# Kernel tuning notes

Measured on AMD Instinct MI355X. Metric: run time of the kernel, lower is better.

The kernel has to match this reference:

```python
import jax, jax.numpy as jnp
import numpy as np

PI = float(np.pi)
C = jnp.complex64
N = 10  # qubits

def m2(a, b, c, d):
    a, b, c, d = jnp.broadcast_arrays(*(jnp.asarray(v, C) for v in (a, b, c, d)))
    return jnp.stack([jnp.stack([a, b], -1), jnp.stack([c, d], -1)], -2)

def rx_mat(t):
    c = jnp.cos(t / 2); s = jnp.sin(t / 2)
    return m2(c, -1j * s, -1j * s, c)

def ry_mat(t):
    c = jnp.cos(t / 2); s = jnp.sin(t / 2)
    return m2(c, -s, s, c)

def rz_mat(t):
    return m2(jnp.exp(-0.5j * t), 0.0, 0.0, jnp.exp(0.5j * t))

def ps_mat(t):
    return m2(1.0, 0.0, 0.0, jnp.exp(1j * t))

def rot_mat(phi, theta, omega):
    c = jnp.cos(theta / 2); s = jnp.sin(theta / 2)
    return m2(jnp.exp(-0.5j * (phi + omega)) * c,
              -jnp.exp(0.5j * (phi - omega)) * s,
              jnp.exp(-0.5j * (phi - omega)) * s,
              jnp.exp(0.5j * (phi + omega)) * c)

def u2_mat(phi, lam):
    r = 1.0 / np.sqrt(2.0)
    return m2(r, -r * jnp.exp(1j * lam), r * jnp.exp(1j * phi), r * jnp.exp(1j * (phi + lam)))

def u3_mat(theta, phi, lam):
    c = jnp.cos(theta / 2); s = jnp.sin(theta / 2)
    return m2(c, -jnp.exp(1j * lam) * s, jnp.exp(1j * phi) * s, jnp.exp(1j * (phi + lam)) * c)

def controlled(U):
    sh = U.shape[:-2]
    I2 = jnp.broadcast_to(jnp.eye(2, dtype=C), sh + (2, 2))
    Z2 = jnp.zeros(sh + (2, 2), C)
    return jnp.concatenate([jnp.concatenate([I2, Z2], -1), jnp.concatenate([Z2, U], -1)], -2)

Y_M = jnp.array([[0, -1j], [1j, 0]], C)
S_M = jnp.array([[1, 0], [0, 1j]], C)
T_M = jnp.array([[1, 0], [0, np.exp(1j * np.pi / 4)]], C)
SX_M = 0.5 * jnp.array([[1 + 1j, 1 - 1j], [1 - 1j, 1 + 1j]], C)
CNOT_M = jnp.array(np.eye(4)[[0, 1, 3, 2]], C)
CZ_M = jnp.array(np.diag([1.0, 1.0, 1.0, -1.0]), C)
CY_M = jnp.array([[1, 0, 0, 0], [0, 1, 0, 0], [0, 0, 0, -1j], [0, 0, 1j, 0]], C)
SWAP_M = jnp.array(np.eye(4)[[0, 2, 1, 3]], C)
CSWAP_M = jnp.array(np.eye(8)[[0, 1, 2, 3, 4, 6, 5, 7]], C)
TOFF_M = jnp.array(np.eye(8)[[0, 1, 2, 3, 4, 5, 7, 6]], C)
CX12_M = jnp.array(np.eye(4)[[0, 1, 3, 2]], C)  # qubitunitary [[1,0,0,0],[0,1,0,0],[0,0,0,1],[0,0,1,0]]

def apply_gate(state, U, wires):
    # state: [B] + [2]*N ; U: [2^k,2^k] or [B,2^k,2^k]
    B = state.shape[0]
    k = len(wires)
    axes = tuple(w + 1 for w in wires)
    s = jnp.moveaxis(state, axes, tuple(range(1, 1 + k)))
    sh = s.shape
    s = s.reshape(B, 2 ** k, -1)
    U = jnp.asarray(U, s.dtype)
    if U.ndim == 2:
        s = jnp.einsum('ij,bjr->bir', U, s)
    else:
        s = jnp.einsum('bij,bjr->bir', U, s)
    return jnp.moveaxis(s.reshape(sh), tuple(range(1, 1 + k)), axes)

def multirz(state, theta, wires):
    # diagonal exp(-i theta/2 * Z...Z) phase
    z = jnp.array([1.0, -1.0], jnp.float32)
    sign = jnp.ones((1,) * (N + 1), jnp.float32)
    for w in wires:
        shp = [1] * (N + 1); shp[w + 1] = 2
        sign = sign * z.reshape(shp)
    theta = jnp.reshape(jnp.asarray(theta), (-1,) + (1,) * N)
    return state * jnp.exp(-0.5j * theta * sign)

def net(x, w1, b1, w2, b2, fw1, fb1, fw2, fb2):
    dn = ('NCHW', 'OIHW', 'NCHW')
    h = jax.lax.conv_general_dilated(x, w1, (1, 1), 'VALID', dimension_numbers=dn)
    h = jax.nn.relu(h + b1[None, :, None, None])
    h = jax.lax.conv_general_dilated(h, w2, (1, 1), 'VALID', dimension_numbers=dn)
    h = jax.nn.relu(h + b2[None, :, None, None])
    h = jax.lax.reduce_window(h, -jnp.inf, jax.lax.max, (1, 1, 2, 2), (1, 1, 2, 2), 'VALID')
    h = h.reshape(h.shape[0], -1)  # [B, 9216]
    h = jax.nn.relu(h @ fw1.T + fb1)
    h = h @ fw2.T + fb2
    return jax.nn.sigmoid(h) * (2.0 * PI)  # angles in [0, 2pi], dropout in eval mode

def run_circuit(ang, q_rx, q_rz3, q_ps6, q_rot7, q_mrz8, q_crx9, q_cry10, q_crz11, q_u2, q_u3):
    B = ang.shape[0]
    state = jnp.zeros((B, 2 ** N), C).at[:, 0].set(1.0).reshape((B,) + (2,) * N)
    for k in range(N):  # TrainableOpAll(RX)
        state = apply_gate(state, rx_mat(q_rx[k]), (k,))
    for k in range(N):  # OpAll(RY) + repeated rx(wire0, x[:,0])
        state = apply_gate(state, ry_mat(ang[:, k]), (k,))
        state = apply_gate(state, rx_mat(ang[:, 0]), (0,))
    for k in range(N - 1):  # TQAll CNOT ring
        state = apply_gate(state, CNOT_M, (k, k + 1))
    state = apply_gate(state, CNOT_M, (N - 1, 0))
    state = apply_gate(state, rx_mat(ang[:, 1]), (1,))
    state = apply_gate(state, rx_mat(jnp.float32(-PI / 4)), (5,))  # q_layer2 fixed
    state = apply_gate(state, ry_mat(ang[:, 2]), (2,))
    state = apply_gate(state, rz_mat(ang[:, 3]), (3,))
    state = apply_gate(state, S_M, (4,))
    state = apply_gate(state, T_M, (5,))
    state = apply_gate(state, rz_mat(q_rz3[0]), (6,))
    state = apply_gate(state, SX_M, (7,))
    # q_device1 (3-wire) ops do not affect the output -> omitted
    state = apply_gate(state, CZ_M, (0, 5))
    state = apply_gate(state, CNOT_M, (0, 5))
    state = apply_gate(state, CY_M, (0, 5))
    state = apply_gate(state, CY_M, (3, 8))
    state = apply_gate(state, SWAP_M, (2, 3))
    state = apply_gate(state, CSWAP_M, (4, 5, 6))
    state = apply_gate(state, TOFF_M, (8, 5, 0))
    state = apply_gate(state, ps_mat(q_ps6[0]), (8,))
    state = apply_gate(state, ps_mat(ang[:, 7]), (7,))
    state = apply_gate(state, rot_mat(q_rot7[0], q_rot7[1], q_rot7[2]), (4,))
    state = apply_gate(state, rot_mat(ang[:, 6], ang[:, 7], ang[:, 8]), (5,))
    state = multirz(state, q_mrz8[0], (2, 3, 4, 5, 6))
    state = multirz(state, ang[:, 5], (3, 4, 6, 7, 8))
    state = apply_gate(state, controlled(rx_mat(ang[:, 6])), (0, 1))
    state = apply_gate(state, controlled(rx_mat(q_crx9[0])), (4, 5))
    state = apply_gate(state, controlled(ry_mat(ang[:, 6])), (0, 1))
    state = apply_gate(state, controlled(ry_mat(q_cry10[0])), (4, 5))
    state = apply_gate(state, controlled(rz_mat(ang[:, 6])), (0, 1))
    state = apply_gate(state, controlled(rz_mat(q_crz11[0])), (4, 5))
    state = apply_gate(state, controlled(rot_mat(jnp.float32(-PI / 4), jnp.float32(PI / 4), jnp.float32(PI / 2))), (5, 6))
    state = apply_gate(state, controlled(rot_mat(ang[:, 5], ang[:, 6], ang[:, 7])), (7, 8))
    state = apply_gate(state, ps_mat(jnp.float32(PI / 7)), (1,))  # U1 == PhaseShift
    state = apply_gate(state, ps_mat(ang[:, 9]), (2,))
    state = apply_gate(state, u2_mat(q_u2[0], q_u2[1]), (8,))
    state = apply_gate(state, u2_mat(ang[:, 0], ang[:, 1]), (4,))
    state = apply_gate(state, u3_mat(q_u3[0], q_u3[1], q_u3[2]), (5,))
    state = apply_gate(state, u3_mat(ang[:, 4], ang[:, 5], ang[:, 6]), (5,))
    # q_layer16 QubitUnitary is identity -> no-op
    state = apply_gate(state, CX12_M, (1, 2))
    red = tuple(range(1, N + 1))
    evs = [jnp.real(jnp.sum(jnp.conj(state) * apply_gate(state, Y_M, (w,)), axis=red)) for w in range(N)]
    return jnp.stack(evs, 1)  # [B, 10]

def setup_inputs():
    key = jax.random.key(0)
    ks = jax.random.split(key, 16)
    B = 1024
    return {
        'x': jax.random.uniform(ks[0], (B, 1, 28, 28), jnp.float32),
        'conv1_w': jax.random.normal(ks[1], (32, 1, 3, 3), jnp.float32) * 0.2,
        'conv1_b': jnp.zeros((32,), jnp.float32),
        'conv2_w': jax.random.normal(ks[2], (64, 32, 3, 3), jnp.float32) * 0.05,
        'conv2_b': jnp.zeros((64,), jnp.float32),
        'fc1_w': jax.random.normal(ks[3], (128, 9216), jnp.float32) * 0.01,
        'fc1_b': jnp.zeros((128,), jnp.float32),
        'fc2_w': jax.random.normal(ks[4], (10, 128), jnp.float32) * 0.08,
        'fc2_b': jnp.zeros((10,), jnp.float32),
        'q_rx': jax.random.uniform(ks[5], (10,), jnp.float32, 0.0, 2 * PI),
        'q_rz3': jax.random.uniform(ks[6], (1,), jnp.float32, 0.0, 2 * PI),
        'q_ps6': jax.random.uniform(ks[7], (1,), jnp.float32, 0.0, 2 * PI),
        'q_rot7': jax.random.uniform(ks[8], (3,), jnp.float32, 0.0, 2 * PI),
        'q_mrz8': jax.random.uniform(ks[9], (1,), jnp.float32, 0.0, 2 * PI),
        'q_crx9': jax.random.uniform(ks[10], (1,), jnp.float32, 0.0, 2 * PI),
        'q_cry10': jax.random.uniform(ks[11], (1,), jnp.float32, 0.0, 2 * PI),
        'q_crz11': jax.random.uniform(ks[12], (1,), jnp.float32, 0.0, 2 * PI),
        'q_u2_14': jnp.array([PI / 7, PI / 8.8], jnp.float32),
        'q_u3_15': jax.random.uniform(ks[13], (3,), jnp.float32, 0.0, 2 * PI),
    }

def reference(x, conv1_w, conv1_b, conv2_w, conv2_b, fc1_w, fc1_b, fc2_w, fc2_b,
              q_rx, q_rz3, q_ps6, q_rot7, q_mrz8, q_crx9, q_cry10, q_crz11, q_u2_14, q_u3_15):
    ang = net(x, conv1_w, conv1_b, conv2_w, conv2_b, fc1_w, fc1_b, fc2_w, fc2_b)
    ev = run_circuit(ang, q_rx, q_rz3, q_ps6, q_rot7, q_mrz8, q_crx9, q_cry10, q_crz11, q_u2_14, q_u3_15)
    return jax.nn.log_softmax(ev, axis=1)
```

## Files before the change

kernel.cpp:

```cpp
#include <hip/hip_runtime.h>
#include <hip/hip_bf16.h>

#define PI_F 3.14159265358979323846f

__global__ void Static_82300163326800_kernel() {}

typedef _Float16 f16x8 __attribute__((ext_vector_type(8)));
typedef _Float16 f16x4 __attribute__((ext_vector_type(4)));
typedef float f32x4 __attribute__((ext_vector_type(4)));

struct M2 { float2 m00, m01, m10, m11; };

__device__ __forceinline__ float2 cmul2(float2 a, float2 b) {
    return make_float2(a.x*b.x - a.y*b.y, a.x*b.y + a.y*b.x);
}
__device__ __forceinline__ float2 cadd2(float2 a, float2 b) {
    return make_float2(a.x+b.x, a.y+b.y);
}
__device__ __forceinline__ float2 shx(float2 v, int m) {
    return make_float2(__shfl_xor(v.x, m), __shfl_xor(v.y, m));
}
__device__ __forceinline__ M2 m2mul(M2 b, M2 a) {
    return { cadd2(cmul2(b.m00,a.m00), cmul2(b.m01,a.m10)),
             cadd2(cmul2(b.m00,a.m01), cmul2(b.m01,a.m11)),
             cadd2(cmul2(b.m10,a.m00), cmul2(b.m11,a.m10)),
             cadd2(cmul2(b.m10,a.m01), cmul2(b.m11,a.m11)) };
}
__device__ __forceinline__ M2 mrx(float th) {
    float s, c; __sincosf(0.5f * th, &s, &c);
    return { make_float2(c,0.f), make_float2(0.f,-s), make_float2(0.f,-s), make_float2(c,0.f) };
}
__device__ __forceinline__ M2 mry(float th) {
    float s, c; __sincosf(0.5f * th, &s, &c);
    return { make_float2(c,0.f), make_float2(-s,0.f), make_float2(s,0.f), make_float2(c,0.f) };
}
__device__ __forceinline__ M2 mrot(float phi, float th, float om) {
    float s, c;  __sincosf(0.5f * th, &s, &c);
    float sa, ca; __sincosf(0.5f * (phi + om), &sa, &ca);
    float sd, cd; __sincosf(0.5f * (phi - om), &sd, &cd);
    return { make_float2(ca*c, -sa*c), make_float2(-cd*s, -sd*s),
             make_float2(cd*s, -sd*s), make_float2(ca*c,  sa*c) };
}
__device__ __forceinline__ M2 mu2(float phi, float lam) {
    const float r = 0.7071067811865476f;
    float sl, cl;   __sincosf(lam, &sl, &cl);
    float sp, cp;   __sincosf(phi, &sp, &cp);
    float spl, cpl; __sincosf(phi + lam, &spl, &cpl);
    return { make_float2(r,0.f), make_float2(-r*cl,-r*sl),
             make_float2(r*cp, r*sp), make_float2(r*cpl, r*spl) };
}
__device__ __forceinline__ M2 mu3(float th, float phi, float lam) {
    float s, c;     __sincosf(0.5f * th, &s, &c);
    float sl, cl;   __sincosf(lam, &sl, &cl);
    float sp, cp;   __sincosf(phi, &sp, &cp);
    float spl, cpl; __sincosf(phi + lam, &spl, &cpl);
    return { make_float2(c,0.f), make_float2(-cl*s,-sl*s),
             make_float2(cp*s, sp*s), make_float2(cpl*c, spl*c) };
}


__device__ __forceinline__ void applyL(float2* s, M2 m, int lane, int q) {
    const int bitv = (lane >> q) & 1;
    const float2 cA = bitv ? m.m11 : m.m00;
    const float2 cB = bitv ? m.m10 : m.m01;
    float ox[16], oy[16];
#pragma unroll
    for (int r = 0; r < 16; ++r) {
        ox[r] = __shfl_xor(s[r].x, 1 << q);
        oy[r] = __shfl_xor(s[r].y, 1 << q);
    }
#pragma unroll
    for (int r = 0; r < 16; ++r)
        s[r] = make_float2(cA.x*s[r].x - cA.y*s[r].y + cB.x*ox[r] - cB.y*oy[r],
                           cA.x*s[r].y + cA.y*s[r].x + cB.x*oy[r] + cB.y*ox[r]);
}
template<int P>
__device__ __forceinline__ void applyR(float2* s, M2 m) {
#pragma unroll
    for (int r0 = 0; r0 < 16; ++r0) {
        if (r0 & (1 << P)) continue;
        const int r1 = r0 | (1 << P);
        float2 a = s[r0], d = s[r1];
        s[r0] = cadd2(cmul2(m.m00, a), cmul2(m.m01, d));
        s[r1] = cadd2(cmul2(m.m10, a), cmul2(m.m11, d));
    }
}
__device__ __forceinline__ void diagL(float2* s, float2 d0, float2 d1, int lane, int q) {
    const int bitv = (lane >> q) & 1;
    const float2 f = bitv ? d1 : d0;
#pragma unroll
    for (int r = 0; r < 16; ++r) s[r] = cmul2(f, s[r]);
}
template<int P>
__device__ __forceinline__ void diagR(float2* s, float2 d0, float2 d1) {
#pragma unroll
    for (int r = 0; r < 16; ++r) {
        const float2 f = (r & (1 << P)) ? d1 : d0;
        s[r] = cmul2(f, s[r]);
    }
}
__device__ __forceinline__ void cnotLL(float2* s, int lane, int qc, int qw) {
    const int cb = (lane >> qc) & 1;
    float ox[16], oy[16];
#pragma unroll
    for (int r = 0; r < 16; ++r) {
        ox[r] = __shfl_xor(s[r].x, 1 << qw);
        oy[r] = __shfl_xor(s[r].y, 1 << qw);
    }
#pragma unroll
    for (int r = 0; r < 16; ++r)
        s[r] = cb ? make_float2(ox[r], oy[r]) : s[r];
}
__device__ __forceinline__ void capplyLL(float2* s, M2 m, int lane, int qc, int qw) {
    const int cb = (lane >> qc) & 1, tb = (lane >> qw) & 1;
    float2 cA = tb ? m.m11 : m.m00;
    float2 cB = tb ? m.m10 : m.m01;
    cA = cb ? cA : make_float2(1.f, 0.f);
    cB = cb ? cB : make_float2(0.f, 0.f);
    float ox[16], oy[16];
#pragma unroll
    for (int r = 0; r < 16; ++r) {
        ox[r] = __shfl_xor(s[r].x, 1 << qw);
        oy[r] = __shfl_xor(s[r].y, 1 << qw);
    }
#pragma unroll
    for (int r = 0; r < 16; ++r)
        s[r] = make_float2(cA.x*s[r].x - cA.y*s[r].y + cB.x*ox[r] - cB.y*oy[r],
                           cA.x*s[r].y + cA.y*s[r].x + cB.x*oy[r] + cB.y*ox[r]);
}
__device__ __forceinline__ void cdiagLL(float2* s, float2 d0, float2 d1, int lane, int qc, int qw) {
    const int cb = (lane >> qc) & 1, tb = (lane >> qw) & 1;
    float2 f = tb ? d1 : d0;
    f = cb ? f : make_float2(1.f, 0.f);
#pragma unroll
    for (int r = 0; r < 16; ++r) s[r] = cmul2(f, s[r]);
}
template<int P>
__device__ __forceinline__ void capplyRL(float2* s, M2 m, int lane, int qc) {
    const int cb = (lane >> qc) & 1;
#pragma unroll
    for (int r0 = 0; r0 < 16; ++r0) {
        if (r0 & (1 << P)) continue;
        const int r1 = r0 | (1 << P);
        float2 a = s[r0], d = s[r1];
        float2 na = cadd2(cmul2(m.m00, a), cmul2(m.m01, d));
        float2 nd = cadd2(cmul2(m.m10, a), cmul2(m.m11, d));
        s[r0] = cb ? na : a;
        s[r1] = cb ? nd : d;
    }
}

__global__ __launch_bounds__(256, 1) void circuit_wave(
    const float* __restrict__ ang_g,
    const float* __restrict__ q_rx, const float* __restrict__ q_rz3,
    const float* __restrict__ q_ps6, const float* __restrict__ q_rot7,
    const float* __restrict__ q_mrz8, const float* __restrict__ q_crx9,
    const float* __restrict__ q_cry10, const float* __restrict__ q_crz11,
    const float* __restrict__ q_u2, const float* __restrict__ q_u3,
    float* __restrict__ out)
{
    const int t = threadIdx.x, lane = t & 63, wv = t >> 6;
    const int b = blockIdx.x * 4 + wv;
    float ang[10];
#pragma unroll
    for (int j = 0; j < 10; ++j) ang[j] = ang_g[b * 10 + j];

    float2 s[16];
#pragma unroll
    for (int r = 0; r < 16; ++r) s[r] = make_float2(0.f, 0.f);
    if (lane == 0) s[0].x = 1.f;

    applyL(s, mrx(q_rx[0]), lane, 5);
    applyL(s, mrx(q_rx[1]), lane, 4);
    applyL(s, mrx(q_rx[2]), lane, 3);
    applyL(s, mrx(q_rx[3]), lane, 2);
    applyL(s, mrx(q_rx[4]), lane, 1);
    applyL(s, mrx(q_rx[5]), lane, 0);
    applyR<3>(s, mrx(q_rx[6]));
    applyR<2>(s, mrx(q_rx[7]));
    applyR<1>(s, mrx(q_rx[8]));
    applyR<0>(s, mrx(q_rx[9]));
    applyL(s, mry(ang[0]), lane, 5);
    applyL(s, mry(ang[1]), lane, 4);
    applyL(s, mry(ang[2]), lane, 3);
    applyL(s, mry(ang[3]), lane, 2);
    applyL(s, mry(ang[4]), lane, 1);
    applyL(s, mry(ang[5]), lane, 0);
    applyR<3>(s, mry(ang[6]));
    applyR<2>(s, mry(ang[7]));
    applyR<1>(s, mry(ang[8]));
    applyR<0>(s, mry(ang[9]));
    applyL(s, mrx(10.f * ang[0]), lane, 5);
    cnotLL(s, lane, 5, 4);
    cnotLL(s, lane, 4, 3);
    cnotLL(s, lane, 3, 2);
    cnotLL(s, lane, 2, 1);
    cnotLL(s, lane, 1, 0);
    {
        const int cb = lane & 1;
#pragma unroll
        for (int r0 = 0; r0 < 8; ++r0) {
            float2 a = s[r0], d = s[r0 + 8];
            s[r0] = cb ? d : a; s[r0 + 8] = cb ? a : d;
        }
    }
    {
        float2 u;
        u = s[8];  s[8]  = s[12]; s[12] = u;
        u = s[9];  s[9]  = s[13]; s[13] = u;
        u = s[10]; s[10] = s[14]; s[14] = u;
        u = s[11]; s[11] = s[15]; s[15] = u;
    }
    {
        float2 u;
        u = s[4];  s[4]  = s[6];  s[6]  = u;
        u = s[5];  s[5]  = s[7];  s[7]  = u;
        u = s[12]; s[12] = s[14]; s[14] = u;
        u = s[13]; s[13] = s[15]; s[15] = u;
    }
    {
        float2 u;
        u = s[2];  s[2]  = s[3];  s[3]  = u;
        u = s[6];  s[6]  = s[7];  s[7]  = u;
        u = s[10]; s[10] = s[11]; s[11] = u;
        u = s[14]; s[14] = s[15]; s[15] = u;
    }
    {
        float ox[8], oy[8];
#pragma unroll
        for (int k = 0; k < 8; ++k) {
            ox[k] = __shfl_xor(s[2*k+1].x, 32);
            oy[k] = __shfl_xor(s[2*k+1].y, 32);
        }
#pragma unroll
        for (int k = 0; k < 8; ++k) s[2*k+1] = make_float2(ox[k], oy[k]);
    }

    applyL(s, mrx(ang[1]), lane, 4);
    applyL(s, mrx(-PI_F / 4.f), lane, 0);
    applyL(s, mry(ang[2]), lane, 3);
    { float sn, cs; __sincosf(0.5f * ang[3], &sn, &cs);
      diagL(s, make_float2(cs,-sn), make_float2(cs,sn), lane, 2); }
    diagL(s, make_float2(1.f,0.f), make_float2(0.f,1.f), lane, 1);
    diagL(s, make_float2(1.f,0.f),
          make_float2(0.7071067811865476f, 0.7071067811865476f), lane, 0);
    { float sn, cs; __sincosf(0.5f * q_rz3[0], &sn, &cs);
      diagR<3>(s, make_float2(cs,-sn), make_float2(cs,sn)); }
    { M2 m = { make_float2(0.5f,0.5f), make_float2(0.5f,-0.5f),
               make_float2(0.5f,-0.5f), make_float2(0.5f,0.5f) };
      applyR<2>(s, m); }
    {
        const int cb = (lane >> 5) & 1;
#pragma unroll
        for (int r = 0; r < 16; ++r)
            s[r] = cb ? make_float2(s[r].y, -s[r].x) : s[r];
    }
    {
        const int cb = (lane >> 2) & 1;
#pragma unroll
        for (int r0 = 0; r0 < 16; ++r0) {
            if (r0 & 2) continue;
            const int r1 = r0 | 2;
            float2 a = s[r0], d = s[r1];
            float2 na = make_float2(d.y, -d.x);
            float2 nd = make_float2(-a.y, a.x);
            s[r0] = cb ? na : a; s[r1] = cb ? nd : d;
        }
    }
    {
        const int pr = ((lane >> 3) & 1) ^ ((lane >> 2) & 1);
        float ox[16], oy[16];
#pragma unroll
        for (int r = 0; r < 16; ++r) {
            ox[r] = __shfl_xor(s[r].x, 12);
            oy[r] = __shfl_xor(s[r].y, 12);
        }
#pragma unroll
        for (int r = 0; r < 16; ++r)
            s[r] = pr ? make_float2(ox[r], oy[r]) : s[r];
    }
    {
        float ox[16], oy[16];
#pragma unroll
        for (int r = 0; r < 16; ++r) {
            ox[r] = __shfl_xor(s[r ^ 8].x, 1);
            oy[r] = __shfl_xor(s[r ^ 8].y, 1);
        }
        const int cb = (lane >> 1) & 1, lb = lane & 1;
#pragma unroll
        for (int r = 0; r < 16; ++r) {
            const int pr = cb & ((r & 8) ? (1 - lb) : lb);
            s[r] = pr ? make_float2(ox[r], oy[r]) : s[r];
        }
    }
    {
        const int lb = lane & 1;
        float ox[8], oy[8];
        const int idx8[8] = {2,3,6,7,10,11,14,15};
#pragma unroll
        for (int k = 0; k < 8; ++k) {
            ox[k] = __shfl_xor(s[idx8[k]].x, 32);
            oy[k] = __shfl_xor(s[idx8[k]].y, 32);
        }
#pragma unroll
        for (int k = 0; k < 8; ++k)
            s[idx8[k]] = lb ? make_float2(ox[k], oy[k]) : s[idx8[k]];
    }
    { float sn, cs; __sincosf(q_ps6[0], &sn, &cs);
      diagR<1>(s, make_float2(1.f,0.f), make_float2(cs,sn)); }
    { float sn, cs; __sincosf(ang[7], &sn, &cs);
      diagR<2>(s, make_float2(1.f,0.f), make_float2(cs,sn)); }
    applyL(s, mrot(q_rot7[0], q_rot7[1], q_rot7[2]), lane, 1);
    applyL(s, mrot(ang[6], ang[7], ang[8]), lane, 0);
    {
        float sh, ch; __sincosf(0.5f * q_mrz8[0], &sh, &ch);
        const int lp = __popc(lane & 0xF) & 1;
        const float sg0 = lp ? sh : -sh;
#pragma unroll
        for (int r = 0; r < 16; ++r) {
            const float sg = (r & 8) ? -sg0 : sg0;
            float2 a = s[r];
            s[r] = make_float2(ch*a.x - sg*a.y, ch*a.y + sg*a.x);
        }
    }
    {
        float sh, ch; __sincosf(0.5f * ang[5], &sh, &ch);
        const int lp = __popc(lane & 6) & 1;
        const float sg0 = lp ? sh : -sh;
#pragma unroll
        for (int r = 0; r < 16; ++r) {
            const int rp = __popc(r & 14) & 1;
            const float sg = rp ? -sg0 : sg0;
            float2 a = s[r];
            s[r] = make_float2(ch*a.x - sg*a.y, ch*a.y + sg*a.x);
        }
    }
    capplyLL(s, mrx(ang[6]), lane, 5, 4);
    capplyLL(s, mrx(q_crx9[0]), lane, 1, 0);
    capplyLL(s, mry(ang[6]), lane, 5, 4);
    capplyLL(s, mry(q_cry10[0]), lane, 1, 0);
    { float sn, cs; __sincosf(0.5f * ang[6], &sn, &cs);
      cdiagLL(s, make_float2(cs,-sn), make_float2(cs,sn), lane, 5, 4); }
    { float sn, cs; __sincosf(0.5f * q_crz11[0], &sn, &cs);
      cdiagLL(s, make_float2(cs,-sn), make_float2(cs,sn), lane, 1, 0); }
    capplyRL<3>(s, mrot(-PI_F/4.f, PI_F/4.f, PI_F/2.f), lane, 0);
    {
        M2 m = mrot(ang[5], ang[6], ang[7]);
        const int idx4[4] = {4, 5, 12, 13};
#pragma unroll
        for (int k = 0; k < 4; ++k) {
            const int r0 = idx4[k], r1 = r0 | 2;
            float2 a = s[r0], d = s[r1];
            s[r0] = cadd2(cmul2(m.m00, a), cmul2(m.m01, d));
            s[r1] = cadd2(cmul2(m.m10, a), cmul2(m.m11, d));
        }
    }
    { float sn, cs; __sincosf(PI_F / 7.f, &sn, &cs);
      diagL(s, make_float2(1.f,0.f), make_float2(cs,sn), lane, 4); }
    { float sn, cs; __sincosf(ang[9], &sn, &cs);
      diagL(s, make_float2(1.f,0.f), make_float2(cs,sn), lane, 3); }
    applyR<1>(s, mu2(q_u2[0], q_u2[1]));
    applyL(s, mu2(ang[0], ang[1]), lane, 1);
    applyL(s, m2mul(mu3(ang[4], ang[5], ang[6]),
                    mu3(q_u3[0], q_u3[1], q_u3[2])), lane, 0);
    cnotLL(s, lane, 4, 3);

    float ev[10];
#pragma unroll
    for (int w = 0; w < 6; ++w) {
        const int q = 5 - w;
        const int bitv = (lane >> q) & 1;
        float ox[16], oy[16];
#pragma unroll
        for (int r = 0; r < 16; ++r) {
            ox[r] = __shfl_xor(s[r].x, 1 << q);
            oy[r] = __shfl_xor(s[r].y, 1 << q);
        }
        float acc = 0.f;
#pragma unroll
        for (int r = 0; r < 16; ++r)
            acc += s[r].x * oy[r] - s[r].y * ox[r];
        ev[w] = bitv ? 0.f : 2.f * acc;
    }
#pragma unroll
    for (int w = 6; w < 10; ++w) {
        const int P = 9 - w;
        float acc = 0.f;
#pragma unroll
        for (int r0 = 0; r0 < 16; ++r0) {
            if (r0 & (1 << P)) continue;
            const int r1 = r0 | (1 << P);
            acc += s[r0].x * s[r1].y - s[r0].y * s[r1].x;
        }
        ev[w] = 2.f * acc;
    }
#pragma unroll
    for (int w = 0; w < 10; ++w) {
        float v = ev[w];
        v += __shfl_down(v, 32); v += __shfl_down(v, 16); v += __shfl_down(v, 8);
        v += __shfl_down(v, 4);  v += __shfl_down(v, 2);  v += __shfl_down(v, 1);
        ev[w] = v;
    }
    if (lane == 0) {
        float mx = ev[0];
#pragma unroll
        for (int i = 1; i < 10; ++i) mx = fmaxf(mx, ev[i]);
        float ss = 0.f;
#pragma unroll
        for (int i = 0; i < 10; ++i) ss += expf(ev[i] - mx);
        const float ls = logf(ss);
#pragma unroll
        for (int i = 0; i < 10; ++i) out[b * 10 + i] = ev[i] - mx - ls;
    }
}

__global__ __launch_bounds__(256) void prep_w2(
    const float* __restrict__ w2, _Float16* __restrict__ w2t)
{
    int idx = blockIdx.x * 256 + threadIdx.x;
    if (idx < 18432) {
        int oc = idx / 288, r = idx - oc * 288;
        int s = r >> 5, ic = r & 31;
        w2t[idx] = (_Float16)w2[oc * 288 + ic * 9 + s];
    }
}

__global__ __launch_bounds__(256) void prep_fw1(
    const float* __restrict__ fw1, _Float16* __restrict__ out)
{
    int i = blockIdx.x * 256 + threadIdx.x;
    if (i < 294912) {
        float4 v = ((const float4*)fw1)[i];
        f16x4 o = { (_Float16)v.x, (_Float16)v.y, (_Float16)v.z, (_Float16)v.w };
        *(f16x4*)(out + i * 4) = o;
    }
}

__global__ __launch_bounds__(256, 2) void convnet_mfma(
    const float* __restrict__ x, const float* __restrict__ w1, const float* __restrict__ b1,
    const _Float16* __restrict__ w2t, const float* __restrict__ b2,
    _Float16* __restrict__ flat)
{
    __shared__ float xs[784];
    __shared__ float w1s[288];
    __shared__ __align__(16) _Float16 h1t[676 * 40];
    const int n = blockIdx.x, t = threadIdx.x;
    const int lane = t & 63, wv = t >> 6;
    const int m = lane & 15, quad = lane >> 4;

    for (int i = t; i < 784; i += 256) xs[i] = x[n * 784 + i];
    for (int i = t; i < 288; i += 256) w1s[i] = w1[i];

    f16x8 bq[9][4];
#pragma unroll
    for (int s = 0; s < 9; ++s)
#pragma unroll
        for (int nt = 0; nt < 4; ++nt)
            bq[s][nt] = *(const f16x8*)(w2t + (nt * 16 + m) * 288 + s * 32 + quad * 8);

    __syncthreads();

    {
        const int ic = t & 31, j = t >> 5;
        float wr[9];
#pragma unroll
        for (int k = 0; k < 9; ++k) wr[k] = w1s[ic * 9 + k];
        const float bb = b1[ic];
        for (int pg = j; pg < 13; pg += 8) {
            const int y0 = 2 * pg;
            float p0[4], p1[4];
#pragma unroll
            for (int k = 0; k < 4; ++k) {
                p0[k] = xs[(y0 + k) * 28];
                p1[k] = xs[(y0 + k) * 28 + 1];
            }
            for (int xx = 0; xx < 26; ++xx) {
                float n2[4];
#pragma unroll
                for (int k = 0; k < 4; ++k) n2[k] = xs[(y0 + k) * 28 + xx + 2];
                float s0 = bb, s1 = bb;
#pragma unroll
                for (int ky = 0; ky < 3; ++ky) {
                    s0 += p0[ky] * wr[3*ky] + p1[ky] * wr[3*ky+1] + n2[ky] * wr[3*ky+2];
                    s1 += p0[ky+1] * wr[3*ky] + p1[ky+1] * wr[3*ky+1] + n2[ky+1] * wr[3*ky+2];
                }
                h1t[(y0 * 26 + xx) * 40 + ic]       = (_Float16)fmaxf(s0, 0.f);
                h1t[((y0 + 1) * 26 + xx) * 40 + ic] = (_Float16)fmaxf(s1, 0.f);
#pragma unroll
                for (int k = 0; k < 4; ++k) { p0[k] = p1[k]; p1[k] = n2[k]; }
            }
        }
    }
    __syncthreads();

    float bb2[4];
#pragma unroll
    for (int nt = 0; nt < 4; ++nt) bb2[nt] = b2[nt * 16 + m];

    _Float16* outp = flat + (size_t)n * 9216;

    for (int q = 0; q < 9; ++q) {
        const int mt = wv + q * 4;
        const int a = mt / 3, b3 = mt - a * 3;
        const int y0 = 2 * a + (m & 1), x0 = 8 * b3 + (m >> 1);
        f32x4 acc[4] = {};
#pragma unroll
        for (int s = 0; s < 9; ++s) {
            const int ky = s / 3, kx = s - ky * 3;
            f16x8 af = *(const f16x8*)&h1t[((y0 + ky) * 26 + x0 + kx) * 40 + quad * 8];
#pragma unroll
            for (int nt = 0; nt < 4; ++nt)
                acc[nt] = __builtin_amdgcn_mfma_f32_16x16x32_f16(af, bq[s][nt], acc[nt], 0, 0, 0);
        }
        const int pooled_idx = a * 12 + 4 * b3 + quad;
#pragma unroll
        for (int nt = 0; nt < 4; ++nt) {
            float v = fmaxf(fmaxf(acc[nt][0], acc[nt][1]), fmaxf(acc[nt][2], acc[nt][3]));
            outp[(nt * 16 + m) * 144 + pooled_idx] = (_Float16)fmaxf(v + bb2[nt], 0.f);
        }
    }
}

__global__ __launch_bounds__(256) void fc1_mfma(
    const _Float16* __restrict__ A, const _Float16* __restrict__ B, float* __restrict__ part)
{
    const int m0 = blockIdx.x * 64, n0 = blockIdx.y * 64, kb = blockIdx.z;
    const int t = threadIdx.x, lane = t & 63, wv = t >> 6;
    const int r = lane & 15, quad = lane >> 4;
    const _Float16* ap = A + (size_t)(m0 + wv * 16 + r) * 9216 + kb * 576 + quad * 8;
    const _Float16* bp = B + (size_t)(n0 + r) * 9216 + kb * 576 + quad * 8;
    f32x4 acc[4] = {};
    for (int ks = 0; ks < 576; ks += 32) {
        f16x8 af = *(const f16x8*)(ap + ks);
#pragma unroll
        for (int nt = 0; nt < 4; ++nt) {
            f16x8 bfr = *(const f16x8*)(bp + (size_t)nt * 16 * 9216 + ks);
            acc[nt] = __builtin_amdgcn_mfma_f32_16x16x32_f16(af, bfr, acc[nt], 0, 0, 0);
        }
    }
    float* pp = part + (size_t)kb * 131072 + (size_t)(m0 + wv * 16 + quad * 4) * 128 + n0 + r;
#pragma unroll
    for (int nt = 0; nt < 4; ++nt)
#pragma unroll
        for (int reg = 0; reg < 4; ++reg)
            pp[reg * 128 + nt * 16] = acc[nt][reg];
}

__global__ __launch_bounds__(128) void fc2_kernel(
    const float* __restrict__ part, const float* __restrict__ fb1,
    const float* __restrict__ fw2, const float* __restrict__ fb2, float* __restrict__ angO)
{
    __shared__ float h[128];
    const int b = blockIdx.x, t = threadIdx.x;
    float s = fb1[t];
#pragma unroll
    for (int kb = 0; kb < 16; ++kb) s += part[(size_t)kb * 131072 + b * 128 + t];
    h[t] = fmaxf(s, 0.f);
    __syncthreads();
    if (t < 10) {
        float d = fb2[t];
#pragma unroll 16
        for (int k = 0; k < 128; ++k) d += h[k] * fw2[t * 128 + k];
        angO[b * 10 + t] = 6.283185307179586f / (1.f + expf(-d));
    }
}

__device__ __forceinline__ int ins1(int x, int p) {
    return ((x >> p) << (p + 1)) | (x & ((1 << p) - 1));
}
__device__ __forceinline__ void apply1(float2* st, int t, int w, M2 m) {
    int p = 9 - w;
    int i0 = ins1(t, p), i1 = i0 | (1 << p);
    float2 a = st[i0], d = st[i1];
    st[i0] = cadd2(cmul2(m.m00, a), cmul2(m.m01, d));
    st[i1] = cadd2(cmul2(m.m10, a), cmul2(m.m11, d));
}
__device__ __forceinline__ void diag1(float2* st, int t, int w, float2 d0, float2 d1) {
    int p = 9 - w;
    int i0 = ins1(t, p), i1 = i0 | (1 << p);
    st[i0] = cmul2(d0, st[i0]);
    st[i1] = cmul2(d1, st[i1]);
}
__device__ __forceinline__ void capply1(float2* st, int t, int c, int w, M2 m) {
    if (t < 256) {
        int pc = 9 - c, pw = 9 - w;
        int pl = pc < pw ? pc : pw, ph = pc + pw - pl;
        int base = ins1(ins1(t, pl), ph) | (1 << pc);
        int i0 = base, i1 = base | (1 << pw);
        float2 a = st[i0], d = st[i1];
        st[i0] = cadd2(cmul2(m.m00, a), cmul2(m.m01, d));
        st[i1] = cadd2(cmul2(m.m10, a), cmul2(m.m11, d));
    }
}
__device__ __forceinline__ void cdiag1(float2* st, int t, int c, int w, float2 d0, float2 d1) {
    if (t < 256) {
        int pc = 9 - c, pw = 9 - w;
        int pl = pc < pw ? pc : pw, ph = pc + pw - pl;
        int base = ins1(ins1(t, pl), ph) | (1 << pc);
        st[base] = cmul2(d0, st[base]);
        st[base | (1 << pw)] = cmul2(d1, st[base | (1 << pw)]);
    }
}
__device__ __forceinline__ void cnotg(float2* st, int t, int c, int w) {
    if (t < 256) {
        int pc = 9 - c, pw = 9 - w;
        int pl = pc < pw ? pc : pw, ph = pc + pw - pl;
        int base = ins1(ins1(t, pl), ph) | (1 << pc);
        int i1 = base | (1 << pw);
        float2 a = st[base]; st[base] = st[i1]; st[i1] = a;
    }
}
__device__ __forceinline__ void czg(float2* st, int t, int c, int w) {
    if (t < 256) {
        int pc = 9 - c, pw = 9 - w;
        int pl = pc < pw ? pc : pw, ph = pc + pw - pl;
        int i = ins1(ins1(t, pl), ph) | (1 << pc) | (1 << pw);
        st[i] = make_float2(-st[i].x, -st[i].y);
    }
}
__device__ __forceinline__ void swapg(float2* st, int t, int a, int b_) {
    if (t < 256) {
        int pa = 9 - a, pb = 9 - b_;
        int pl = pa < pb ? pa : pb, ph = pa + pb - pl;
        int base = ins1(ins1(t, pl), ph);
        int iA = base | (1 << pa), iB = base | (1 << pb);
        float2 u = st[iA]; st[iA] = st[iB]; st[iB] = u;
    }
}
__device__ __forceinline__ void cswap456f(float2* st, int t) {
    if (t < 128) {
        int base = ins1(ins1(ins1(t, 3), 4), 5) | (1 << 5);
        int iA = base | (1 << 4), iB = base | (1 << 3);
        float2 u = st[iA]; st[iA] = st[iB]; st[iB] = u;
    }
}
__device__ __forceinline__ void toff850f(float2* st, int t) {
    if (t < 128) {
        int base = ins1(ins1(ins1(t, 1), 4), 9) | (1 << 1) | (1 << 4);
        int i1 = base | (1 << 9);
        float2 u = st[base]; st[base] = st[i1]; st[i1] = u;
    }
}
__device__ __forceinline__ void mrzg(float2* st, int t, int mask, float th) {
    float sh, ch; __sincosf(0.5f * th, &sh, &ch);
#pragma unroll
    for (int q = 0; q < 2; ++q) {
        int i = t + q * 512;
        float sg = (__popc(i & mask) & 1) ? sh : -sh;
        float2 a = st[i];
        st[i] = make_float2(ch*a.x - sg*a.y, ch*a.y + sg*a.x);
    }
}
__device__ __forceinline__ void run_circ(
    float2* st, float (*red)[10], float* evs, int t, const float* ang,
    const float* q_rx, const float* q_rz3, const float* q_ps6, const float* q_rot7,
    const float* q_mrz8, const float* q_crx9, const float* q_cry10, const float* q_crz11,
    const float* q_u2, const float* q_u3, float* outf)
{
    st[t] = make_float2(t == 0 ? 1.f : 0.f, 0.f);
    st[t + 512] = make_float2(0.f, 0.f);
#pragma unroll
    for (int k = 0; k < 10; ++k) { M2 m = mrx(q_rx[k]); __syncthreads(); apply1(st, t, k, m); }
    {
        M2 mx0 = mrx(ang[0]);
#pragma unroll
        for (int k = 0; k < 10; ++k) {
            M2 m = mry(ang[k]); __syncthreads(); apply1(st, t, k, m);
            __syncthreads(); apply1(st, t, 0, mx0);
        }
    }
#pragma unroll
    for (int k = 0; k < 9; ++k) { __syncthreads(); cnotg(st, t, k, k + 1); }
    __syncthreads(); cnotg(st, t, 9, 0);
    { M2 m = mrx(ang[1]);      __syncthreads(); apply1(st, t, 1, m); }
    { M2 m = mrx(-PI_F / 4.f); __syncthreads(); apply1(st, t, 5, m); }
    { M2 m = mry(ang[2]);      __syncthreads(); apply1(st, t, 2, m); }
    { float s, c; __sincosf(0.5f * ang[3], &s, &c);
      __syncthreads(); diag1(st, t, 3, make_float2(c,-s), make_float2(c,s)); }
    __syncthreads(); diag1(st, t, 4, make_float2(1.f,0.f), make_float2(0.f,1.f));
    __syncthreads(); diag1(st, t, 5, make_float2(1.f,0.f),
                           make_float2(0.7071067811865476f, 0.7071067811865476f));
    { float s, c; __sincosf(0.5f * q_rz3[0], &s, &c);
      __syncthreads(); diag1(st, t, 6, make_float2(c,-s), make_float2(c,s)); }
    { M2 m = { make_float2(0.5f,0.5f), make_float2(0.5f,-0.5f),
               make_float2(0.5f,-0.5f), make_float2(0.5f,0.5f) };
      __syncthreads(); apply1(st, t, 7, m); }
    __syncthreads(); czg(st, t, 0, 5);
    __syncthreads(); cnotg(st, t, 0, 5);
    { M2 y = { make_float2(0.f,0.f), make_float2(0.f,-1.f),
               make_float2(0.f,1.f), make_float2(0.f,0.f) };
      __syncthreads(); capply1(st, t, 0, 5, y);
      __syncthreads(); capply1(st, t, 3, 8, y); }
    __syncthreads(); swapg(st, t, 2, 3);
    __syncthreads(); cswap456f(st, t);
    __syncthreads(); toff850f(st, t);
    { float s, c; __sincosf(q_ps6[0], &s, &c);
      __syncthreads(); diag1(st, t, 8, make_float2(1.f,0.f), make_float2(c,s)); }
    { float s, c; __sincosf(ang[7], &s, &c);
      __syncthreads(); diag1(st, t, 7, make_float2(1.f,0.f), make_float2(c,s)); }
    { M2 m = mrot(q_rot7[0], q_rot7[1], q_rot7[2]); __syncthreads(); apply1(st, t, 4, m); }
    { M2 m = mrot(ang[6], ang[7], ang[8]);          __syncthreads(); apply1(st, t, 5, m); }
    __syncthreads(); mrzg(st, t, 0xF8, q_mrz8[0]);
    __syncthreads(); mrzg(st, t, 0x6E, ang[5]);
    { M2 m = mrx(ang[6]);      __syncthreads(); capply1(st, t, 0, 1, m); }
    { M2 m = mrx(q_crx9[0]);   __syncthreads(); capply1(st, t, 4, 5, m); }
    { M2 m = mry(ang[6]);      __syncthreads(); capply1(st, t, 0, 1, m); }
    { M2 m = mry(q_cry10[0]);  __syncthreads(); capply1(st, t, 4, 5, m); }
    { float s, c; __sincosf(0.5f * ang[6], &s, &c);
      __syncthreads(); cdiag1(st, t, 0, 1, make_float2(c,-s), make_float2(c,s)); }
    { float s, c; __sincosf(0.5f * q_crz11[0], &s, &c);
      __syncthreads(); cdiag1(st, t, 4, 5, make_float2(c,-s), make_float2(c,s)); }
    { M2 m = mrot(-PI_F/4.f, PI_F/4.f, PI_F/2.f); __syncthreads(); capply1(st, t, 5, 6, m); }
    { M2 m = mrot(ang[5], ang[6], ang[7]);        __syncthreads(); capply1(st, t, 7, 8, m); }
    { float s, c; __sincosf(PI_F/7.f, &s, &c);
      __syncthreads(); diag1(st, t, 1, make_float2(1.f,0.f), make_float2(c,s)); }
    { float s, c; __sincosf(ang[9], &s, &c);
      __syncthreads(); diag1(st, t, 2, make_float2(1.f,0.f), make_float2(c,s)); }
    { M2 m = mu2(q_u2[0], q_u2[1]); __syncthreads(); apply1(st, t, 8, m); }
    { M2 m = mu2(ang[0], ang[1]);   __syncthreads(); apply1(st, t, 4, m); }
    { M2 m = mu3(q_u3[0], q_u3[1], q_u3[2]); __syncthreads(); apply1(st, t, 5, m); }
    { M2 m = mu3(ang[4], ang[5], ang[6]);    __syncthreads(); apply1(st, t, 5, m); }
    __syncthreads(); cnotg(st, t, 1, 2);
    __syncthreads();
    float loc[10];
#pragma unroll
    for (int w = 0; w < 10; ++w) {
        int p = 9 - w;
        int i0 = ins1(t, p), i1 = i0 | (1 << p);
        float2 a = st[i0], c = st[i1];
        loc[w] = 2.f * (a.x * c.y - a.y * c.x);
    }
    int lane = t & 63, wvv = t >> 6;
#pragma unroll
    for (int w = 0; w < 10; ++w) {
        float v = loc[w];
        v += __shfl_down(v, 32); v += __shfl_down(v, 16); v += __shfl_down(v, 8);
        v += __shfl_down(v, 4);  v += __shfl_down(v, 2);  v += __shfl_down(v, 1);
        if (lane == 0) red[wvv][w] = v;
    }
    __syncthreads();
    if (t < 10) {
        float e = 0.f;
#pragma unroll
        for (int i = 0; i < 8; ++i) e += red[i][t];
        evs[t] = e;
    }
    __syncthreads();
    if (t < 10) {
        float mx = evs[0];
#pragma unroll
        for (int i = 1; i < 10; ++i) mx = fmaxf(mx, evs[i]);
        float ss = 0.f;
#pragma unroll
        for (int i = 0; i < 10; ++i) ss += expf(evs[i] - mx);
        outf[t] = evs[t] - mx - logf(ss);
    }
}
template <int NT>
__device__ __forceinline__ void conv_stage(
    float* buf, int n, int t,
    const float* __restrict__ x, const float* __restrict__ w1, const float* __restrict__ b1,
    const float* __restrict__ w2, const float* __restrict__ b2)
{
    float* xs  = buf;
    float* w1s = buf + 784;
    float* h1s = buf + 1072;
    float* w2s = buf + 1748;
    const int ocq = t / 24, r = t - ocq * 24;
    const bool active = (t < 384);
    for (int i = t; i < 784; i += NT) xs[i] = x[n * 784 + i];
    for (int i = t; i < 288; i += NT) w1s[i] = w1[i];
    float acc[4][24];
#pragma unroll
    for (int j = 0; j < 4; ++j)
#pragma unroll
        for (int xo = 0; xo < 24; ++xo) acc[j][xo] = 0.f;
    for (int ic = 0; ic < 32; ++ic) {
        __syncthreads();
        float bb1 = b1[ic];
        for (int i = t; i < 676; i += NT) {
            int yy = i / 26, xx = i - yy * 26;
            const float* xp = xs + yy * 28 + xx;
            const float* wp = w1s + ic * 9;
            float s = bb1;
#pragma unroll
            for (int ky = 0; ky < 3; ++ky)
#pragma unroll
                for (int kx = 0; kx < 3; ++kx)
                    s += xp[ky * 28 + kx] * wp[ky * 3 + kx];
            h1s[i] = fmaxf(s, 0.f);
        }
        for (int i = t; i < 576; i += NT) {
            int oc = i / 9, k = i - oc * 9;
            w2s[i] = w2[oc * 288 + ic * 9 + k];
        }
        __syncthreads();
        if (active) {
            float wr[4][9];
#pragma unroll
            for (int j = 0; j < 4; ++j)
#pragma unroll
                for (int k = 0; k < 9; ++k)
                    wr[j][k] = w2s[(ocq * 4 + j) * 9 + k];
            float c0[3], c1[3];
#pragma unroll
            for (int q = 0; q < 3; ++q) { c0[q] = h1s[(r + q) * 26]; c1[q] = h1s[(r + q) * 26 + 1]; }
#pragma unroll
            for (int xo = 0; xo < 24; ++xo) {
                float c2[3];
#pragma unroll
                for (int q = 0; q < 3; ++q) c2[q] = h1s[(r + q) * 26 + xo + 2];
#pragma unroll
                for (int j = 0; j < 4; ++j) {
                    acc[j][xo] += wr[j][0]*c0[0] + wr[j][1]*c1[0] + wr[j][2]*c2[0]
                                + wr[j][3]*c0[1] + wr[j][4]*c1[1] + wr[j][5]*c2[1]
                                + wr[j][6]*c0[2] + wr[j][7]*c1[2] + wr[j][8]*c2[2];
                }
#pragma unroll
                for (int q = 0; q < 3; ++q) { c0[q] = c1[q]; c1[q] = c2[q]; }
            }
        }
    }
    __syncthreads();
    if (active && (r & 1)) {
#pragma unroll
        for (int j = 0; j < 4; ++j) {
            int oc = ocq * 4 + j;
            float bb = b2[oc];
#pragma unroll
            for (int px = 0; px < 12; ++px) {
                float v0 = fmaxf(acc[j][2*px]   + bb, 0.f);
                float v1 = fmaxf(acc[j][2*px+1] + bb, 0.f);
                buf[oc * 144 + (r >> 1) * 12 + px] = fmaxf(v0, v1);
            }
        }
    }
    __syncthreads();
    if (active && !(r & 1)) {
#pragma unroll
        for (int j = 0; j < 4; ++j) {
            int oc = ocq * 4 + j;
            float bb = b2[oc];
#pragma unroll
            for (int px = 0; px < 12; ++px) {
                float v0 = fmaxf(acc[j][2*px]   + bb, 0.f);
                float v1 = fmaxf(acc[j][2*px+1] + bb, 0.f);
                int idx = oc * 144 + (r >> 1) * 12 + px;
                buf[idx] = fmaxf(fmaxf(v0, v1), buf[idx]);
            }
        }
    }
    __syncthreads();
}
__global__ __launch_bounds__(512) void fused_kernel(
    const float* __restrict__ x, const float* __restrict__ w1, const float* __restrict__ b1,
    const float* __restrict__ w2, const float* __restrict__ b2,
    const float* __restrict__ fw1, const float* __restrict__ fb1,
    const float* __restrict__ fw2, const float* __restrict__ fb2,
    const float* __restrict__ q_rx, const float* __restrict__ q_rz3,
    const float* __restrict__ q_ps6, const float* __restrict__ q_rot7,
    const float* __restrict__ q_mrz8, const float* __restrict__ q_crx9,
    const float* __restrict__ q_cry10, const float* __restrict__ q_crz11,
    const float* __restrict__ q_u2, const float* __restrict__ q_u3,
    float* __restrict__ out)
{
    __shared__ float buf[9216];
    __shared__ float2 st[1024];
    __shared__ float hred[512];
    __shared__ float hvec[128];
    __shared__ float angs[10];
    __shared__ float red[8][10];
    __shared__ float evs[10];
    const int n = blockIdx.x, t = threadIdx.x;
    conv_stage<512>(buf, n, t, x, w1, b1, w2, b2);
    {
        const int j = t >> 2, q = t & 3;
        const float* wrow = fw1 + (size_t)j * 9216 + q * 2304;
        const float* arow = buf + q * 2304;
        float s = 0.f;
        for (int k = 0; k < 2304; k += 4) {
            float4 w = *(const float4*)(wrow + k);
            s += w.x * arow[k] + w.y * arow[k+1] + w.z * arow[k+2] + w.w * arow[k+3];
        }
        hred[t] = s;
    }
    __syncthreads();
    if (t < 128)
        hvec[t] = fmaxf(fb1[t] + hred[t*4] + hred[t*4+1] + hred[t*4+2] + hred[t*4+3], 0.f);
    __syncthreads();
    if (t < 10) {
        float d = fb2[t];
#pragma unroll 16
        for (int k = 0; k < 128; ++k) d += hvec[k] * fw2[t * 128 + k];
        angs[t] = 6.283185307179586f / (1.f + expf(-d));
    }
    __syncthreads();
    run_circ(st, red, evs, t, angs, q_rx, q_rz3, q_ps6, q_rot7, q_mrz8,
             q_crx9, q_cry10, q_crz11, q_u2, q_u3, out + n * 10);
}

extern "C" void kernel_launch(void* const* d_in, const int* in_sizes, int n_in,
                              void* d_out, int out_size, void* d_ws, size_t ws_size,
                              hipStream_t stream)
{
    (void)in_sizes; (void)n_in;
    const float* x    = (const float*)d_in[0];
    const float* w1   = (const float*)d_in[1];
    const float* b1   = (const float*)d_in[2];
    const float* w2   = (const float*)d_in[3];
    const float* b2   = (const float*)d_in[4];
    const float* fw1  = (const float*)d_in[5];
    const float* fb1  = (const float*)d_in[6];
    const float* fw2  = (const float*)d_in[7];
    const float* fb2  = (const float*)d_in[8];
    const float* qrx  = (const float*)d_in[9];
    const float* qrz3 = (const float*)d_in[10];
    const float* qps6 = (const float*)d_in[11];
    const float* qrot7 = (const float*)d_in[12];
    const float* qmrz8 = (const float*)d_in[13];
    const float* qcrx9 = (const float*)d_in[14];
    const float* qcry10 = (const float*)d_in[15];
    const float* qcrz11 = (const float*)d_in[16];
    const float* qu2  = (const float*)d_in[17];
    const float* qu3  = (const float*)d_in[18];
    float* out = (float*)d_out;

    const size_t flat_bytes = (size_t)1024 * 9216 * 2;
    const size_t part_bytes = (size_t)16 * 1024 * 128 * 4;
    const size_t ang_bytes  = (size_t)1024 * 10 * 4;
    const size_t w2t_bytes  = (size_t)18432 * 2;
    const size_t fw1h_bytes = (size_t)128 * 9216 * 2;
    const size_t o_flat = 0;
    const size_t o_part = o_flat + flat_bytes;
    const size_t o_ang  = o_part + part_bytes;
    const size_t o_w2t  = o_ang + ang_bytes;
    const size_t o_fw1h = o_w2t + w2t_bytes;
    const size_t need   = o_fw1h + fw1h_bytes;

    (void)hipGetLastError();

    if (ws_size >= need) {
        _Float16* flat = (_Float16*)((char*)d_ws + o_flat);
        float*    part = (float*)((char*)d_ws + o_part);
        float*    angb = (float*)((char*)d_ws + o_ang);
        _Float16* w2t  = (_Float16*)((char*)d_ws + o_w2t);
        _Float16* fw1h = (_Float16*)((char*)d_ws + o_fw1h);
        prep_w2<<<72, 256, 0, stream>>>(w2, w2t);
        prep_fw1<<<1152, 256, 0, stream>>>(fw1, fw1h);
        convnet_mfma<<<1024, 256, 0, stream>>>(x, w1, b1, w2t, b2, flat);
        fc1_mfma<<<dim3(16, 2, 16), 256, 0, stream>>>(flat, fw1h, part);
        fc2_kernel<<<1024, 128, 0, stream>>>(part, fb1, fw2, fb2, angb);
        circuit_wave<<<256, 256, 0, stream>>>(angb, qrx, qrz3, qps6, qrot7, qmrz8,
                                              qcrx9, qcry10, qcrz11, qu2, qu3, out);
    } else {
        fused_kernel<<<1024, 512, 0, stream>>>(x, w1, b1, w2, b2, fw1, fb1, fw2, fb2,
                                               qrx, qrz3, qps6, qrot7, qmrz8,
                                               qcrx9, qcry10, qcrz11, qu2, qu3, out);
    }
    if (hipGetLastError() != hipSuccess) {
        (void)hipMemsetAsync(d_out, 0x7F, (size_t)out_size * 2, stream);
    }
}
```

Measured before the change: 190.4 us.

## Fuse fc2 into circuit kernel, merge prep kernels, restructure conv1 per-pixel

The fc2 reduction (summing the fc1 split-K partials, ReLU, the 128->10 dot product and the sigmoid scaling) now runs inside the circuit kernel. Each wave reduces with shuffles across lanes, which removes one launch and the angle buffer round trip. The two weight-prep kernels are merged into a single launch. Conv1 is rewritten so each thread computes 8 channels per pixel from transposed weights held in registers and writes vectorized f16x8 to LDS; this adds register pressure and an extra sync before the MFMA weight loads.

```diff
diff --git a/kernel.cpp b/kernel.cpp
--- a/kernel.cpp
+++ b/kernel.cpp
@@ -151,7 +151,8 @@
 }
 
 __global__ __launch_bounds__(256, 1) void circuit_wave(
-    const float* __restrict__ ang_g,
+    const float* __restrict__ part, const float* __restrict__ fb1,
+    const float* __restrict__ fw2, const float* __restrict__ fb2,
     const float* __restrict__ q_rx, const float* __restrict__ q_rz3,
     const float* __restrict__ q_ps6, const float* __restrict__ q_rot7,
     const float* __restrict__ q_mrz8, const float* __restrict__ q_crx9,
@@ -161,9 +162,22 @@
 {
     const int t = threadIdx.x, lane = t & 63, wv = t >> 6;
     const int b = blockIdx.x * 4 + wv;
+
+    float h0 = fb1[lane], h1 = fb1[lane + 64];
+#pragma unroll
+    for (int kb = 0; kb < 16; ++kb) {
+        h0 += part[(size_t)kb * 131072 + b * 128 + lane];
+        h1 += part[(size_t)kb * 131072 + b * 128 + lane + 64];
+    }
+    h0 = fmaxf(h0, 0.f); h1 = fmaxf(h1, 0.f);
     float ang[10];
 #pragma unroll
-    for (int j = 0; j < 10; ++j) ang[j] = ang_g[b * 10 + j];
+    for (int j = 0; j < 10; ++j) {
+        float v = h0 * fw2[j * 128 + lane] + h1 * fw2[j * 128 + 64 + lane];
+        v += __shfl_xor(v, 1); v += __shfl_xor(v, 2); v += __shfl_xor(v, 4);
+        v += __shfl_xor(v, 8); v += __shfl_xor(v, 16); v += __shfl_xor(v, 32);
+        ang[j] = 6.283185307179586f / (1.f + expf(-(fb2[j] + v)));
+    }
 
     float2 s[16];
 #pragma unroll
@@ -414,25 +428,23 @@
     }
 }
 
-__global__ __launch_bounds__(256) void prep_w2(
+__global__ __launch_bounds__(256) void prep_all(
+    const float* __restrict__ fw1, _Float16* __restrict__ fw1h,
     const float* __restrict__ w2, _Float16* __restrict__ w2t)
 {
-    int idx = blockIdx.x * 256 + threadIdx.x;
-    if (idx < 18432) {
-        int oc = idx / 288, r = idx - oc * 288;
-        int s = r >> 5, ic = r & 31;
-        w2t[idx] = (_Float16)w2[oc * 288 + ic * 9 + s];
-    }
-}
-
-__global__ __launch_bounds__(256) void prep_fw1(
-    const float* __restrict__ fw1, _Float16* __restrict__ out)
-{
-    int i = blockIdx.x * 256 + threadIdx.x;
-    if (i < 294912) {
+    const int blk = blockIdx.x;
+    if (blk < 1152) {
+        int i = blk * 256 + threadIdx.x;
         float4 v = ((const float4*)fw1)[i];
         f16x4 o = { (_Float16)v.x, (_Float16)v.y, (_Float16)v.z, (_Float16)v.w };
-        *(f16x4*)(out + i * 4) = o;
+        *(f16x4*)(fw1h + i * 4) = o;
+    } else {
+        int idx = (blk - 1152) * 256 + threadIdx.x;
+        if (idx < 18432) {
+            int oc = idx / 288, r = idx - oc * 288;
+            int s = r >> 5, ic = r & 31;
+            w2t[idx] = (_Float16)w2[oc * 288 + ic * 9 + s];
+        }
     }
 }
 
@@ -442,14 +454,53 @@
     _Float16* __restrict__ flat)
 {
     __shared__ float xs[784];
-    __shared__ float w1s[288];
+    __shared__ __align__(16) float w1t[288];
     __shared__ __align__(16) _Float16 h1t[676 * 40];
     const int n = blockIdx.x, t = threadIdx.x;
     const int lane = t & 63, wv = t >> 6;
     const int m = lane & 15, quad = lane >> 4;
 
     for (int i = t; i < 784; i += 256) xs[i] = x[n * 784 + i];
-    for (int i = t; i < 288; i += 256) w1s[i] = w1[i];
+    for (int i = t; i < 288; i += 256) {
+        int ic = i / 9, k = i - ic * 9;
+        w1t[k * 32 + ic] = w1[i];
+    }
+    __syncthreads();
+
+    {
+        const int icg = t & 3;
+        float w[9][8];
+#pragma unroll
+        for (int k = 0; k < 9; ++k) {
+            float4 a = *(const float4*)&w1t[k * 32 + icg * 8];
+            float4 bsec = *(const float4*)&w1t[k * 32 + icg * 8 + 4];
+            w[k][0] = a.x; w[k][1] = a.y; w[k][2] = a.z; w[k][3] = a.w;
+            w[k][4] = bsec.x; w[k][5] = bsec.y; w[k][6] = bsec.z; w[k][7] = bsec.w;
+        }
+        float bb[8];
+#pragma unroll
+        for (int j = 0; j < 8; ++j) bb[j] = b1[icg * 8 + j];
+        for (int pix = t >> 2; pix < 676; pix += 64) {
+            const int yy = pix / 26, xx = pix - yy * 26;
+            const float* xp = xs + yy * 28 + xx;
+            float acc[8];
+#pragma unroll
+            for (int j = 0; j < 8; ++j) acc[j] = bb[j];
+#pragma unroll
+            for (int ky = 0; ky < 3; ++ky)
+#pragma unroll
+                for (int kx = 0; kx < 3; ++kx) {
+                    const float xv = xp[ky * 28 + kx];
+                    const int k = ky * 3 + kx;
+#pragma unroll
+                    for (int j = 0; j < 8; ++j) acc[j] += xv * w[k][j];
+                }
+            f16x8 o;
+#pragma unroll
+            for (int j = 0; j < 8; ++j) o[j] = (_Float16)fmaxf(acc[j], 0.f);
+            *(f16x8*)&h1t[pix * 40 + icg * 8] = o;
+        }
+    }
 
     f16x8 bq[9][4];
 #pragma unroll
@@ -458,39 +509,6 @@
         for (int nt = 0; nt < 4; ++nt)
             bq[s][nt] = *(const f16x8*)(w2t + (nt * 16 + m) * 288 + s * 32 + quad * 8);
 
-    __syncthreads();
-
-    {
-        const int ic = t & 31, j = t >> 5;
-        float wr[9];
-#pragma unroll
-        for (int k = 0; k < 9; ++k) wr[k] = w1s[ic * 9 + k];
-        const float bb = b1[ic];
-        for (int pg = j; pg < 13; pg += 8) {
-            const int y0 = 2 * pg;
-            float p0[4], p1[4];
-#pragma unroll
-            for (int k = 0; k < 4; ++k) {
-                p0[k] = xs[(y0 + k) * 28];
-                p1[k] = xs[(y0 + k) * 28 + 1];
-            }
-            for (int xx = 0; xx < 26; ++xx) {
-                float n2[4];
-#pragma unroll
-                for (int k = 0; k < 4; ++k) n2[k] = xs[(y0 + k) * 28 + xx + 2];
-                float s0 = bb, s1 = bb;
-#pragma unroll
-                for (int ky = 0; ky < 3; ++ky) {
-                    s0 += p0[ky] * wr[3*ky] + p1[ky] * wr[3*ky+1] + n2[ky] * wr[3*ky+2];
-                    s1 += p0[ky+1] * wr[3*ky] + p1[ky+1] * wr[3*ky+1] + n2[ky+1] * wr[3*ky+2];
-                }
-                h1t[(y0 * 26 + xx) * 40 + ic]       = (_Float16)fmaxf(s0, 0.f);
-                h1t[((y0 + 1) * 26 + xx) * 40 + ic] = (_Float16)fmaxf(s1, 0.f);
-#pragma unroll
-                for (int k = 0; k < 4; ++k) { p0[k] = p1[k]; p1[k] = n2[k]; }
-            }
-        }
-    }
     __syncthreads();
 
     float bb2[4];
@@ -544,25 +562,6 @@
 #pragma unroll
         for (int reg = 0; reg < 4; ++reg)
             pp[reg * 128 + nt * 16] = acc[nt][reg];
-}
-
-__global__ __launch_bounds__(128) void fc2_kernel(
-    const float* __restrict__ part, const float* __restrict__ fb1,
-    const float* __restrict__ fw2, const float* __restrict__ fb2, float* __restrict__ angO)
-{
-    __shared__ float h[128];
-    const int b = blockIdx.x, t = threadIdx.x;
-    float s = fb1[t];
-#pragma unroll
-    for (int kb = 0; kb < 16; ++kb) s += part[(size_t)kb * 131072 + b * 128 + t];
-    h[t] = fmaxf(s, 0.f);
-    __syncthreads();
-    if (t < 10) {
-        float d = fb2[t];
-#pragma unroll 16
-        for (int k = 0; k < 128; ++k) d += h[k] * fw2[t * 128 + k];
-        angO[b * 10 + t] = 6.283185307179586f / (1.f + expf(-d));
-    }
 }
 
 __device__ __forceinline__ int ins1(int x, int p) {
@@ -927,13 +926,11 @@
 
     const size_t flat_bytes = (size_t)1024 * 9216 * 2;
     const size_t part_bytes = (size_t)16 * 1024 * 128 * 4;
-    const size_t ang_bytes  = (size_t)1024 * 10 * 4;
     const size_t w2t_bytes  = (size_t)18432 * 2;
     const size_t fw1h_bytes = (size_t)128 * 9216 * 2;
     const size_t o_flat = 0;
     const size_t o_part = o_flat + flat_bytes;
-    const size_t o_ang  = o_part + part_bytes;
-    const size_t o_w2t  = o_ang + ang_bytes;
+    const size_t o_w2t  = o_part + part_bytes;
     const size_t o_fw1h = o_w2t + w2t_bytes;
     const size_t need   = o_fw1h + fw1h_bytes;
 
@@ -942,15 +939,13 @@
     if (ws_size >= need) {
         _Float16* flat = (_Float16*)((char*)d_ws + o_flat);
         float*    part = (float*)((char*)d_ws + o_part);
-        float*    angb = (float*)((char*)d_ws + o_ang);
         _Float16* w2t  = (_Float16*)((char*)d_ws + o_w2t);
         _Float16* fw1h = (_Float16*)((char*)d_ws + o_fw1h);
-        prep_w2<<<72, 256, 0, stream>>>(w2, w2t);
-        prep_fw1<<<1152, 256, 0, stream>>>(fw1, fw1h);
+        prep_all<<<1224, 256, 0, stream>>>(fw1, fw1h, w2, w2t);
         convnet_mfma<<<1024, 256, 0, stream>>>(x, w1, b1, w2t, b2, flat);
         fc1_mfma<<<dim3(16, 2, 16), 256, 0, stream>>>(flat, fw1h, part);
-        fc2_kernel<<<1024, 128, 0, stream>>>(part, fb1, fw2, fb2, angb);
-        circuit_wave<<<256, 256, 0, stream>>>(angb, qrx, qrz3, qps6, qrot7, qmrz8,
+        circuit_wave<<<256, 256, 0, stream>>>(part, fb1, fw2, fb2,
+                                              qrx, qrz3, qps6, qrot7, qmrz8,
                                               qcrx9, qcry10, qcrz11, qu2, qu3, out);
     } else {
         fused_kernel<<<1024, 512, 0, stream>>>(x, w1, b1, w2, b2, fw1, fb1, fw2, fb2,
```

Result: slower. 196.1 us (+3.0%).
